# Kernel optimization log

Hardware: AMD Instinct MI355X
Metric: run time of the kernel (lower is better)

## Reference

```python
import jax, jax.numpy as jnp
import numpy as np

N_PARTIAL = 1024  # matches init_kwargs


def setup_inputs() -> dict:
    key = jax.random.key(0)
    k1, k2 = jax.random.split(key)
    B, H, L = 8, 768, 4096
    x = jax.random.normal(k1, (B, H, L), dtype=jnp.float32)
    k = jax.random.normal(k2, (H, L), dtype=jnp.float32)
    return {"x": x, "k": k}


def reference(x, k):
    # FFT-based causal long convolution with low-pass frequency truncation.
    L = x.shape[-1]
    N = 2 * L  # zero-pad to 2L for linear (non-circular) convolution
    x_dtype = x.dtype
    x_f = jnp.fft.rfft(x.astype(jnp.float32), n=N)          # [B, H, N//2+1] complex64
    k_f = jnp.fft.rfft(k.astype(jnp.float32), n=N)          # [H, N//2+1]   complex64
    # zero out all frequency bins >= N_partial // 2 (low-pass truncation of the kernel)
    freqs = jnp.arange(N // 2 + 1)
    k_f = jnp.where(freqs < N_PARTIAL // 2, k_f, jnp.zeros((), dtype=k_f.dtype))
    y_f = x_f * k_f                                          # broadcast over batch
    y = jnp.fft.irfft(y_f, n=N)[..., :L].astype(x_dtype)     # [B, H, L]
    return y
```

## Files before the change

### kernel.cpp

```cpp
#include <hip/hip_runtime.h>
#include <math.h>

#define LSEQ 4096
#define NFFT 8192
#define NF   512
#define NF2  1024
#define NH   768
#define NBH  6144
#define MROWS 6912
#define SPLIT_ROW 3456

typedef __attribute__((ext_vector_type(8))) short short8;
typedef __attribute__((ext_vector_type(4))) float floatx4;

__device__ __forceinline__ unsigned short f2bf(float f) {
    unsigned int u = __float_as_uint(f);
    u += 0x7fff + ((u >> 16) & 1);
    return (unsigned short)(u >> 16);
}

__global__ void build_tables(unsigned short* __restrict__ T1,
                             unsigned short* __restrict__ T2) {
    __shared__ unsigned short tile[64][66];
    const int t = threadIdx.x;
    const int F0 = blockIdx.x * 64;
    const int N0 = blockIdx.y * 64;
#pragma unroll
    for (int i = 0; i < 16; ++i) {
        int r = (t >> 6) + i * 4;
        int c = t & 63;
        int f2 = F0 + r, n = N0 + c;
        int f = f2 >> 1;
        int p = (f * n) & (NFFT - 1);
        float th = (float)p * (float)(2.0 * M_PI / (double)NFFT);
        float s, cc;
        sincosf(th, &s, &cc);
        unsigned short v = f2bf((f2 & 1) ? s : cc);
        T1[(size_t)f2 * LSEQ + n] = v;
        tile[r][c] = v;
    }
    __syncthreads();
#pragma unroll
    for (int i = 0; i < 16; ++i) {
        int r = (t >> 6) + i * 4;
        int c = t & 63;
        T2[(size_t)(N0 + r) * NF2 + F0 + c] = tile[c][r];
    }
}

__global__ void tobf16(const float* __restrict__ x, const float* __restrict__ kk,
                       unsigned short* __restrict__ o) {
    size_t e = ((size_t)blockIdx.x * 256 + threadIdx.x) * 4;
    const size_t XN = (size_t)NBH * LSEQ;
    const float* s = (e < XN) ? (x + e) : (kk + (e - XN));
    float4 v = *(const float4*)s;
    unsigned int lo = (unsigned int)f2bf(v.x) | ((unsigned int)f2bf(v.y) << 16);
    unsigned int hi = (unsigned int)f2bf(v.z) | ((unsigned int)f2bf(v.w) << 16);
    *(uint2*)(o + e) = make_uint2(lo, hi);
}

#define LOADSET(ra0, ra1, rb0, rb1, off)                      \
    ra0 = *(const uint4*)(pa0 + (off));                        \
    ra1 = *(const uint4*)(pa1 + (off));                        \
    rb0 = *(const uint4*)(pb0 + (off));                        \
    rb1 = *(const uint4*)(pb1 + (off));

#define WRITESET(buf, ra0, ra1, rb0, rb1)                      \
    *(uint4*)(As[buf] + q0 * 8) = ra0;                         \
    *(uint4*)(As[buf] + q1 * 8) = ra1;                         \
    *(uint4*)(Bs[buf] + q0 * 8) = rb0;                         \
    *(uint4*)(Bs[buf] + q1 * 8) = rb1;

#define COMPUTE(buf)                                                          \
    {                                                                         \
        short8 af[4], bfv[4];                                                 \
        _Pragma("unroll")                                                     \
        for (int i = 0; i < 4; ++i)                                           \
            af[i] = *(const short8*)(As[buf] + (wm + 16 * i + lr) * 32 + lq * 8); \
        _Pragma("unroll")                                                     \
        for (int j = 0; j < 4; ++j)                                           \
            bfv[j] = *(const short8*)(Bs[buf] + (wn + 16 * j + lr) * 32 + lq * 8); \
        _Pragma("unroll")                                                     \
        for (int i = 0; i < 4; ++i)                                           \
            _Pragma("unroll")                                                 \
            for (int j = 0; j < 4; ++j)                                       \
                acc[i][j] = __builtin_amdgcn_mfma_f32_16x16x32_bf16(          \
                    af[i], bfv[j], acc[i][j], 0, 0, 0);                       \
    }

__global__ __launch_bounds__(256) void gemm_bt(
    const unsigned short* __restrict__ A,
    const unsigned short* __restrict__ B,
    float* __restrict__ C,
    float* __restrict__ P1a,
    float* __restrict__ P1b,
    int gx, int gy,
    int N, int ldk, int Ksub)
{
    __shared__ __align__(16) unsigned short As[2][128 * 32];
    __shared__ __align__(16) unsigned short Bs[2][128 * 32];
    const int t = threadIdx.x;
    const int w = t >> 6, l = t & 63;

    const int nwg = gridDim.x;
    const int bid = blockIdx.x;
    const int swz = (bid & 7) * (nwg >> 3) + (bid >> 3);
    const int bx = swz % gx;
    const int rem = swz / gx;
    const int by = rem % gy;
    const int bz = rem / gy;

    const int m0 = by * 128, n0 = bx * 128;
    const int wm = (w >> 1) * 64, wn = (w & 1) * 64;
    const int lq = l >> 4, lr = l & 15;
    const int kbase = bz * Ksub;

    floatx4 acc[4][4];
#pragma unroll
    for (int i = 0; i < 4; ++i)
#pragma unroll
        for (int j = 0; j < 4; ++j)
            acc[i][j] = (floatx4){0.f, 0.f, 0.f, 0.f};

    const int q0 = t, q1 = t + 256;
    const int r0 = q0 >> 2, e0 = (q0 & 3) * 8;
    const int r1 = q1 >> 2, e1 = (q1 & 3) * 8;
    const unsigned short* pa0 = A + (size_t)(m0 + r0) * ldk + e0 + kbase;
    const unsigned short* pa1 = A + (size_t)(m0 + r1) * ldk + e1 + kbase;
    const unsigned short* pb0 = B + (size_t)(n0 + r0) * ldk + e0 + kbase;
    const unsigned short* pb1 = B + (size_t)(n0 + r1) * ldk + e1 + kbase;

    uint4 xa0, xa1, xb0, xb1;
    uint4 ya0, ya1, yb0, yb1;

    LOADSET(xa0, xa1, xb0, xb1, 0)
    WRITESET(0, xa0, xa1, xb0, xb1)
    LOADSET(ya0, ya1, yb0, yb1, 32)
    __syncthreads();

    const int T = Ksub >> 5;
    for (int tt = 0; tt + 4 <= T; tt += 2) {
        LOADSET(xa0, xa1, xb0, xb1, (tt + 2) * 32)
        COMPUTE(0)
        WRITESET(1, ya0, ya1, yb0, yb1)
        __syncthreads();
        LOADSET(ya0, ya1, yb0, yb1, (tt + 3) * 32)
        COMPUTE(1)
        WRITESET(0, xa0, xa1, xb0, xb1)
        __syncthreads();
    }
    COMPUTE(0)
    WRITESET(1, ya0, ya1, yb0, yb1)
    __syncthreads();
    COMPUTE(1)

    float* Cb;
    if (bz == 0) {
        Cb = C;
    } else {
        Cb = (m0 < SPLIT_ROW) ? P1a : (P1b - (size_t)SPLIT_ROW * N);
    }
#pragma unroll
    for (int i = 0; i < 4; ++i)
#pragma unroll
        for (int j = 0; j < 4; ++j)
#pragma unroll
            for (int r = 0; r < 4; ++r) {
                int row = m0 + wm + 16 * i + lq * 4 + r;
                int col = n0 + wn + 16 * j + lr;
                Cb[(size_t)row * N + col] = acc[i][j][r];
            }
}

__global__ void combine(const float* __restrict__ C1,
                        const float* __restrict__ P1a,
                        const float* __restrict__ P1b,
                        unsigned short* __restrict__ AB) {
    int idx = blockIdx.x * blockDim.x + threadIdx.x;
    int bh = idx >> 9;
    int f = idx & (NF - 1);
    int h = bh % NH;
    const float* xc = C1 + (size_t)bh * NF2 + 2 * f;
    const float* xp = (bh < SPLIT_ROW)
        ? (P1a + (size_t)bh * NF2 + 2 * f)
        : (P1b + (size_t)(bh - SPLIT_ROW) * NF2 + 2 * f);
    const int kr = NBH + h;
    const float* kc = C1 + (size_t)kr * NF2 + 2 * f;
    const float* kp = P1b + (size_t)(kr - SPLIT_ROW) * NF2 + 2 * f;
    float Xre = xc[0] + xp[0], Xim = -(xc[1] + xp[1]);
    float Kre = kc[0] + kp[0], Kim = -(kc[1] + kp[1]);
    float s = (f == 0 ? 1.0f : 2.0f) * (1.0f / (float)NFFT);
    float Av = s * (Xre * Kre - Xim * Kim);
    float Bv = -(s * (Xre * Kim + Xim * Kre));
    unsigned int packed = (unsigned int)f2bf(Av) | ((unsigned int)f2bf(Bv) << 16);
    *(unsigned int*)(AB + (size_t)bh * NF2 + 2 * f) = packed;
}

extern "C" void kernel_launch(void* const* d_in, const int* in_sizes, int n_in,
                              void* d_out, int out_size, void* d_ws, size_t ws_size,
                              hipStream_t stream) {
    const float* x = (const float*)d_in[0];
    const float* k = (const float*)d_in[1];
    float* y = (float*)d_out;

    unsigned short* T1 = (unsigned short*)d_ws;
    unsigned short* T2 = T1 + (size_t)NF2 * LSEQ;
    unsigned short* AB = T2 + (size_t)LSEQ * NF2;
    float* P1a = (float*)(AB + (size_t)NBH * NF2);

    unsigned short* Abm = (unsigned short*)d_out;
    float* C1 = (float*)((char*)d_out + (size_t)MROWS * LSEQ * 2);
    float* P1b = C1 + (size_t)MROWS * NF2;

    const int blk = 256;
    hipLaunchKernelGGL(build_tables, dim3(NF2 / 64, LSEQ / 64), dim3(blk), 0, stream, T1, T2);
    hipLaunchKernelGGL(tobf16, dim3((MROWS * LSEQ / 4) / blk), dim3(blk), 0, stream, x, k, Abm);
    hipLaunchKernelGGL(gemm_bt, dim3(8 * 54 * 2), dim3(blk), 0, stream,
                       Abm, T1, C1, P1a, P1b, 8, 54, NF2, LSEQ, LSEQ / 2);
    hipLaunchKernelGGL(combine, dim3((NBH * NF) / blk), dim3(blk), 0, stream, C1, P1a, P1b, AB);
    hipLaunchKernelGGL(gemm_bt, dim3(32 * 48), dim3(blk), 0, stream,
                       AB, T2, y, (float*)nullptr, (float*)nullptr, 32, 48, LSEQ, NF2, NF2);
}
```

Before: 343.0 us.

## Replace GEMM with 256x256-tile 8-wave kernel using direct global-to-LDS loads

Rewrites the bf16 MFMA GEMM to use 256x256 output tiles with 512 threads, a K-step of 64, and global_load_lds to stream tiles straight into LDS with an XOR swizzle that avoids bank conflicts. Prefetch of the next stage is interleaved with four MFMA phases, and s_setprio raises priority during the math. The larger tile is meant to cut global traffic per FLOP and the cost of staging through registers. The trade-off is fewer workgroups (216 and 384), which may leave CUs underused on the split-K first GEMM, plus more barriers. The split row for the partial buffer changes to match the 256-row tile boundary.

```diff
diff --git a/kernel.cpp b/kernel.cpp
--- a/kernel.cpp
+++ b/kernel.cpp
@@ -8,7 +8,7 @@
 #define NH   768
 #define NBH  6144
 #define MROWS 6912
-#define SPLIT_ROW 3456
+#define SPLIT_ROW 3584
 
 typedef __attribute__((ext_vector_type(8))) short short8;
 typedef __attribute__((ext_vector_type(4))) float floatx4;
@@ -17,6 +17,12 @@
     unsigned int u = __float_as_uint(f);
     u += 0x7fff + ((u >> 16) & 1);
     return (unsigned short)(u >> 16);
+}
+
+__device__ __forceinline__ void gld16(const unsigned short* g, const unsigned short* l) {
+    __builtin_amdgcn_global_load_lds(
+        (const __attribute__((address_space(1))) void*)g,
+        (__attribute__((address_space(3))) void*)l, 16, 0, 0);
 }
 
 __global__ void build_tables(unsigned short* __restrict__ T1,
@@ -59,115 +65,116 @@
     *(uint2*)(o + e) = make_uint2(lo, hi);
 }
 
-#define LOADSET(ra0, ra1, rb0, rb1, off)                      \
-    ra0 = *(const uint4*)(pa0 + (off));                        \
-    ra1 = *(const uint4*)(pa1 + (off));                        \
-    rb0 = *(const uint4*)(pb0 + (off));                        \
-    rb1 = *(const uint4*)(pb1 + (off));
-
-#define WRITESET(buf, ra0, ra1, rb0, rb1)                      \
-    *(uint4*)(As[buf] + q0 * 8) = ra0;                         \
-    *(uint4*)(As[buf] + q1 * 8) = ra1;                         \
-    *(uint4*)(Bs[buf] + q0 * 8) = rb0;                         \
-    *(uint4*)(Bs[buf] + q1 * 8) = rb1;
-
-#define COMPUTE(buf)                                                          \
-    {                                                                         \
-        short8 af[4], bfv[4];                                                 \
-        _Pragma("unroll")                                                     \
-        for (int i = 0; i < 4; ++i)                                           \
-            af[i] = *(const short8*)(As[buf] + (wm + 16 * i + lr) * 32 + lq * 8); \
-        _Pragma("unroll")                                                     \
-        for (int j = 0; j < 4; ++j)                                           \
-            bfv[j] = *(const short8*)(Bs[buf] + (wn + 16 * j + lr) * 32 + lq * 8); \
-        _Pragma("unroll")                                                     \
-        for (int i = 0; i < 4; ++i)                                           \
-            _Pragma("unroll")                                                 \
-            for (int j = 0; j < 4; ++j)                                       \
-                acc[i][j] = __builtin_amdgcn_mfma_f32_16x16x32_bf16(          \
-                    af[i], bfv[j], acc[i][j], 0, 0, 0);                       \
-    }
-
-__global__ __launch_bounds__(256) void gemm_bt(
+__global__ __launch_bounds__(512) void gemm8(
     const unsigned short* __restrict__ A,
     const unsigned short* __restrict__ B,
     float* __restrict__ C,
     float* __restrict__ P1a,
     float* __restrict__ P1b,
-    int gx, int gy,
-    int N, int ldk, int Ksub)
+    int gx, int gy, int N, int ldk, int Ksub)
 {
-    __shared__ __align__(16) unsigned short As[2][128 * 32];
-    __shared__ __align__(16) unsigned short Bs[2][128 * 32];
+    __shared__ __align__(16) unsigned short S[2 * 32768];
     const int t = threadIdx.x;
-    const int w = t >> 6, l = t & 63;
-
-    const int nwg = gridDim.x;
-    const int bid = blockIdx.x;
+    const int wid = t >> 6, l = t & 63;
+
+    const int nwg = gridDim.x, bid = blockIdx.x;
     const int swz = (bid & 7) * (nwg >> 3) + (bid >> 3);
     const int bx = swz % gx;
     const int rem = swz / gx;
     const int by = rem % gy;
     const int bz = rem / gy;
 
-    const int m0 = by * 128, n0 = bx * 128;
-    const int wm = (w >> 1) * 64, wn = (w & 1) * 64;
+    const int m0 = by * 256, n0 = bx * 256;
+    const int wr = wid >> 2, wc = wid & 3;
     const int lq = l >> 4, lr = l & 15;
     const int kbase = bz * Ksub;
-
-    floatx4 acc[4][4];
-#pragma unroll
-    for (int i = 0; i < 4; ++i)
+    const int NT = Ksub >> 6;
+
+    const int sx = ((lr >> 2) & 1) << 1;
+    const int s0 = lq ^ sx;
+    const int aoff = (wr * 128 + lr) * 64 + s0 * 8;
+    const int boff = 16384 + (wc * 64 + lr) * 64 + s0 * 8;
+
+    const int gsl = (l & 7) ^ (((l >> 5) & 1) << 1);
+    const unsigned short* pAs = A + (size_t)(m0 + wid * 8 + (l >> 3)) * ldk + kbase + gsl * 8;
+    const unsigned short* pBs = B + (size_t)(n0 + wid * 8 + (l >> 3)) * ldk + kbase + gsl * 8;
+
+    floatx4 acc[8][4];
+#pragma unroll
+    for (int i = 0; i < 8; ++i)
 #pragma unroll
         for (int j = 0; j < 4; ++j)
             acc[i][j] = (floatx4){0.f, 0.f, 0.f, 0.f};
 
-    const int q0 = t, q1 = t + 256;
-    const int r0 = q0 >> 2, e0 = (q0 & 3) * 8;
-    const int r1 = q1 >> 2, e1 = (q1 & 3) * 8;
-    const unsigned short* pa0 = A + (size_t)(m0 + r0) * ldk + e0 + kbase;
-    const unsigned short* pa1 = A + (size_t)(m0 + r1) * ldk + e1 + kbase;
-    const unsigned short* pb0 = B + (size_t)(n0 + r0) * ldk + e0 + kbase;
-    const unsigned short* pb1 = B + (size_t)(n0 + r1) * ldk + e1 + kbase;
-
-    uint4 xa0, xa1, xb0, xb1;
-    uint4 ya0, ya1, yb0, yb1;
-
-    LOADSET(xa0, xa1, xb0, xb1, 0)
-    WRITESET(0, xa0, xa1, xb0, xb1)
-    LOADSET(ya0, ya1, yb0, yb1, 32)
-    __syncthreads();
-
-    const int T = Ksub >> 5;
-    for (int tt = 0; tt + 4 <= T; tt += 2) {
-        LOADSET(xa0, xa1, xb0, xb1, (tt + 2) * 32)
-        COMPUTE(0)
-        WRITESET(1, ya0, ya1, yb0, yb1)
-        __syncthreads();
-        LOADSET(ya0, ya1, yb0, yb1, (tt + 3) * 32)
-        COMPUTE(1)
-        WRITESET(0, xa0, xa1, xb0, xb1)
-        __syncthreads();
+#define STG_A(b, h, kt_)                                                                  \
+    gld16(pAs + (size_t)((h)*128     ) * ldk + (kt_) * 64, S + (b)*32768 +         ((h)*128      + wid*8) * 64); \
+    gld16(pAs + (size_t)((h)*128 + 64) * ldk + (kt_) * 64, S + (b)*32768 +         ((h)*128 + 64 + wid*8) * 64);
+#define STG_B(b, h, kt_)                                                                  \
+    gld16(pBs + (size_t)((h)*128     ) * ldk + (kt_) * 64, S + (b)*32768 + 16384 + ((h)*128      + wid*8) * 64); \
+    gld16(pBs + (size_t)((h)*128 + 64) * ldk + (kt_) * 64, S + (b)*32768 + 16384 + ((h)*128 + 64 + wid*8) * 64);
+
+#define RD_A(Sc, ip)                                                           \
+    _Pragma("unroll") for (int ii = 0; ii < 2; ++ii)                           \
+    _Pragma("unroll") for (int ks = 0; ks < 2; ++ks)                           \
+        aq[ii][ks] = *(const short8*)((Sc) + aoff + 1024 * ((ip) + ii) + 32 * ks);
+#define RD_B(Sc)                                                               \
+    _Pragma("unroll") for (int j = 0; j < 4; ++j)                              \
+    _Pragma("unroll") for (int ks = 0; ks < 2; ++ks)                           \
+        bq[j][ks] = *(const short8*)((Sc) + boff + 1024 * j + 32 * ks);
+#define MM(ip)                                                                 \
+    __builtin_amdgcn_s_setprio(1);                                             \
+    _Pragma("unroll") for (int ii = 0; ii < 2; ++ii)                           \
+    _Pragma("unroll") for (int j = 0; j < 4; ++j)                              \
+    _Pragma("unroll") for (int ks = 0; ks < 2; ++ks)                           \
+        acc[(ip) + ii][j] = __builtin_amdgcn_mfma_f32_16x16x32_bf16(           \
+            aq[ii][ks], bq[j][ks], acc[(ip) + ii][j], 0, 0, 0);                \
+    __builtin_amdgcn_s_setprio(0);
+
+    STG_A(0, 0, 0) STG_A(0, 1, 0) STG_B(0, 0, 0) STG_B(0, 1, 0)
+    asm volatile("s_waitcnt vmcnt(0)" ::: "memory");
+    __builtin_amdgcn_s_barrier();
+
+    short8 aq[2][2], bq[4][2];
+
+    for (int kt = 0; kt < NT; ++kt) {
+        const unsigned short* Sc = S + (size_t)(kt & 1) * 32768;
+        const int bs = (kt & 1) ^ 1;
+        const bool pf = (kt + 1 < NT);
+        if (pf) { STG_A(bs, 0, kt + 1) }
+        if (pf) asm volatile("s_waitcnt vmcnt(2)" ::: "memory");
+        else    asm volatile("s_waitcnt vmcnt(0)" ::: "memory");
+        __builtin_amdgcn_s_barrier();
+        RD_B(Sc) RD_A(Sc, 0)
+        MM(0)
+        __builtin_amdgcn_s_barrier();
+        if (pf) { STG_A(bs, 1, kt + 1) }
+        RD_A(Sc, 2)
+        __builtin_amdgcn_s_barrier();
+        MM(2)
+        __builtin_amdgcn_s_barrier();
+        if (pf) { STG_B(bs, 0, kt + 1) }
+        RD_A(Sc, 4)
+        __builtin_amdgcn_s_barrier();
+        MM(4)
+        __builtin_amdgcn_s_barrier();
+        if (pf) { STG_B(bs, 1, kt + 1) }
+        RD_A(Sc, 6)
+        __builtin_amdgcn_s_barrier();
+        MM(6)
+        __builtin_amdgcn_s_barrier();
     }
-    COMPUTE(0)
-    WRITESET(1, ya0, ya1, yb0, yb1)
-    __syncthreads();
-    COMPUTE(1)
 
     float* Cb;
-    if (bz == 0) {
-        Cb = C;
-    } else {
-        Cb = (m0 < SPLIT_ROW) ? P1a : (P1b - (size_t)SPLIT_ROW * N);
-    }
-#pragma unroll
-    for (int i = 0; i < 4; ++i)
+    if (bz == 0) Cb = C;
+    else Cb = (m0 < SPLIT_ROW) ? P1a : (P1b - (size_t)SPLIT_ROW * N);
+#pragma unroll
+    for (int i = 0; i < 8; ++i)
 #pragma unroll
         for (int j = 0; j < 4; ++j)
 #pragma unroll
             for (int r = 0; r < 4; ++r) {
-                int row = m0 + wm + 16 * i + lq * 4 + r;
-                int col = n0 + wn + 16 * j + lr;
+                int row = m0 + wr * 128 + 16 * i + lq * 4 + r;
+                int col = n0 + wc * 64 + 16 * j + lr;
                 Cb[(size_t)row * N + col] = acc[i][j][r];
             }
 }
@@ -215,9 +222,9 @@
     const int blk = 256;
     hipLaunchKernelGGL(build_tables, dim3(NF2 / 64, LSEQ / 64), dim3(blk), 0, stream, T1, T2);
     hipLaunchKernelGGL(tobf16, dim3((MROWS * LSEQ / 4) / blk), dim3(blk), 0, stream, x, k, Abm);
-    hipLaunchKernelGGL(gemm_bt, dim3(8 * 54 * 2), dim3(blk), 0, stream,
-                       Abm, T1, C1, P1a, P1b, 8, 54, NF2, LSEQ, LSEQ / 2);
+    hipLaunchKernelGGL(gemm8, dim3(4 * 27 * 2), dim3(512), 0, stream,
+                       Abm, T1, C1, P1a, P1b, 4, 27, NF2, LSEQ, LSEQ / 2);
     hipLaunchKernelGGL(combine, dim3((NBH * NF) / blk), dim3(blk), 0, stream, C1, P1a, P1b, AB);
-    hipLaunchKernelGGL(gemm_bt, dim3(32 * 48), dim3(blk), 0, stream,
-                       AB, T2, y, (float*)nullptr, (float*)nullptr, 32, 48, LSEQ, NF2, NF2);
-}
+    hipLaunchKernelGGL(gemm8, dim3(16 * 24), dim3(512), 0, stream,
+                       AB, T2, y, (float*)nullptr, (float*)nullptr, 16, 24, LSEQ, NF2, NF2);
+}
```

Result: faster. 331.5 us (-3.4%).
